# Kernel tuning notes

Hardware: AMD Instinct MI355X
Metric: run time of the kernel (lower is better)

## Reference

```python
import jax, jax.numpy as jnp
import numpy as np

NUM_GRAPHS = 1024

def setup_inputs() -> dict:
    key = jax.random.key(0)
    ks = jax.random.split(key, 6)
    N, E = 500000, 16000000
    x = jax.random.normal(ks[0], (N, 4), dtype=jnp.float32)
    edge_index = jax.random.randint(ks[1], (2, E), 0, N, dtype=jnp.int32)
    batch = jnp.sort(jax.random.randint(ks[2], (N,), 0, NUM_GRAPHS, dtype=jnp.int32))
    eps = jnp.zeros((), dtype=jnp.float32)
    W1 = jax.random.normal(ks[3], (4, 16), dtype=jnp.float32) * 0.5
    b1 = jnp.zeros((16,), dtype=jnp.float32)
    W2 = jax.random.normal(ks[4], (16, 4), dtype=jnp.float32) * 0.25
    b2 = jnp.zeros((4,), dtype=jnp.float32)
    return {"x": x, "edge_index": edge_index, "batch": batch,
            "eps": eps, "W1": W1, "b1": b1, "W2": W2, "b2": b2}

def reference(x, edge_index, batch, eps, W1, b1, W2, b2):
    N = x.shape[0]
    src, dst = edge_index[0], edge_index[1]
    # GINConv aggregation: sum of neighbor (source) features at each target node
    agg = jax.ops.segment_sum(x[src], dst, num_segments=N)  # [N, 4]
    h = (1.0 + eps) * x + agg
    # 2-layer MLP: Lin(4,16) -> ReLU -> Lin(16,4)
    h = jax.nn.relu(h @ W1 + b1) @ W2 + b2
    h = jax.nn.relu(h)
    # global_mean_pool over batch segment ids
    sums = jax.ops.segment_sum(h, batch, num_segments=NUM_GRAPHS)      # [G, 4]
    cnts = jax.ops.segment_sum(jnp.ones((N,), h.dtype), batch, num_segments=NUM_GRAPHS)
    pooled = sums / jnp.maximum(cnts, 1.0)[:, None]
    return jax.nn.log_softmax(pooled, axis=1)
```

## Files before the change

kernel.cpp:

```cpp
#include <hip/hip_runtime.h>

#define NUM_GRAPHS 1024
#define BIN_BITS 10
#define BIN_SIZE (1 << BIN_BITS)
#define EB 8192
#define STH 512
#define EPT 16
#define ATH 1024
#define ACH 8192
#define AEPT (ACH / ATH)

typedef int v4i __attribute__((ext_vector_type(4)));

__device__ inline unsigned bf16_rn(float f) {
    unsigned u = __float_as_uint(f);
    return (u + 0x7FFFu + ((u >> 16) & 1u)) >> 16;
}
__global__ void prep_kernel(const float4* __restrict__ x, uint2* __restrict__ x16,
                            int N, int* __restrict__ cursor,
                            float* __restrict__ gsum, float* __restrict__ gcnt,
                            int cap) {
    int i = blockIdx.x * blockDim.x + threadIdx.x;
    if (i < 512) cursor[i] = i * cap;
    if (i < NUM_GRAPHS * 4) gsum[i] = 0.0f;
    if (i < NUM_GRAPHS) gcnt[i] = 0.0f;
    if (i < N) {
        float4 v = x[i];
        uint2 r;
        r.x = bf16_rn(v.x) | (bf16_rn(v.y) << 16);
        r.y = bf16_rn(v.z) | (bf16_rn(v.w) << 16);
        x16[i] = r;
    }
}

__global__ void __launch_bounds__(STH) bin_scatter(const int* __restrict__ src,
                                                   const int* __restrict__ dst,
                                                   int* __restrict__ packed,
                                                   int* __restrict__ cursor,
                                                   int E, int cap, int nb) {
    __shared__ int shist[512];
    __shared__ int sprefix[513];
    __shared__ int sgbase[512];
    __shared__ int spacked[EB];
    __shared__ unsigned short sbin[EB];
    __shared__ int wsum[8];

    const int t = threadIdx.x;
    const int lane = t & 63;
    const int wave = t >> 6;
    const int b0 = blockIdx.x * EB;
    const int myBase = b0 + t * EPT;

    for (int j = t; j < 512; j += STH) shist[j] = 0;
    __syncthreads();

    int pv[EPT];
    int bl[EPT];
    const bool full = (myBase + EPT <= E);
    if (full) {
#pragma unroll
        for (int v = 0; v < EPT / 4; ++v) {
            int4 d = *(const int4*)(dst + myBase + v * 4);
            int4 s = *(const int4*)(src + myBase + v * 4);
            int bn, lp;
            bn = ((unsigned)d.x) >> BIN_BITS; lp = atomicAdd(&shist[bn], 1);
            pv[v * 4 + 0] = ((d.x & (BIN_SIZE - 1)) << 19) | s.x;
            bl[v * 4 + 0] = (bn << 13) | lp;
            bn = ((unsigned)d.y) >> BIN_BITS; lp = atomicAdd(&shist[bn], 1);
            pv[v * 4 + 1] = ((d.y & (BIN_SIZE - 1)) << 19) | s.y;
            bl[v * 4 + 1] = (bn << 13) | lp;
            bn = ((unsigned)d.z) >> BIN_BITS; lp = atomicAdd(&shist[bn], 1);
            pv[v * 4 + 2] = ((d.z & (BIN_SIZE - 1)) << 19) | s.z;
            bl[v * 4 + 2] = (bn << 13) | lp;
            bn = ((unsigned)d.w) >> BIN_BITS; lp = atomicAdd(&shist[bn], 1);
            pv[v * 4 + 3] = ((d.w & (BIN_SIZE - 1)) << 19) | s.w;
            bl[v * 4 + 3] = (bn << 13) | lp;
        }
    } else {
#pragma unroll
        for (int i = 0; i < EPT; ++i) {
            int e = myBase + i;
            bool ok = e < E;
            int d = ok ? dst[e] : 0;
            int s = ok ? src[e] : 0;
            int bn = ((unsigned)d) >> BIN_BITS;
            int lp = 0;
            if (ok) lp = atomicAdd(&shist[bn], 1);
            pv[i] = ((d & (BIN_SIZE - 1)) << 19) | s;
            bl[i] = ok ? ((bn << 13) | lp) : -1;
        }
    }
    __syncthreads();

    {
        int v = shist[t];
        int inc = v;
#pragma unroll
        for (int off = 1; off < 64; off <<= 1) {
            int u = __shfl_up(inc, off);
            if (lane >= off) inc += u;
        }
        if (lane == 63) wsum[wave] = inc;
        __syncthreads();
        if (t == 0) {
            int acc = 0;
#pragma unroll
            for (int w = 0; w < 8; ++w) { int c = wsum[w]; wsum[w] = acc; acc += c; }
        }
        __syncthreads();
        sprefix[t + 1] = inc + wsum[wave];
        if (t == 0) sprefix[0] = 0;
        if (t < nb && v > 0) sgbase[t] = atomicAdd(&cursor[t], v);
    }
    __syncthreads();

    if (full) {
#pragma unroll
        for (int i = 0; i < EPT; ++i) {
            int bn = ((unsigned)bl[i]) >> 13;
            int lp = bl[i] & 0x1FFF;
            int idx = sprefix[bn] + lp;
            spacked[idx] = pv[i];
            sbin[idx] = (unsigned short)bn;
        }
    } else {
#pragma unroll
        for (int i = 0; i < EPT; ++i) {
            if (bl[i] >= 0) {
                int bn = ((unsigned)bl[i]) >> 13;
                int lp = bl[i] & 0x1FFF;
                int idx = sprefix[bn] + lp;
                spacked[idx] = pv[i];
                sbin[idx] = (unsigned short)bn;
            }
        }
    }
    __syncthreads();

    int cnt = sprefix[nb < 512 ? nb : 512];
    int totE = E - b0; if (totE < 0) totE = 0;
    if (cnt > totE) cnt = totE;
    for (int j = t; j < cnt; j += STH) {
        int bn = sbin[j];
        int pos = sgbase[bn] + (j - sprefix[bn]);
        if (pos < (bn + 1) * cap)
            __builtin_nontemporal_store(spacked[j], &packed[pos]);
    }
}

__global__ void __launch_bounds__(ATH) bin_accum_mlp_pool(
        const float4* __restrict__ x,
        const uint2* __restrict__ x16,
        const int* __restrict__ packed,
        const int* __restrict__ cursor,
        const int* __restrict__ batch,
        const float* __restrict__ eps_p,
        const float* __restrict__ W1, const float* __restrict__ b1,
        const float* __restrict__ W2, const float* __restrict__ b2,
        float* __restrict__ gsum, float* __restrict__ gcnt,
        int N, int cap) {
    __shared__ int srt[ACH];
    __shared__ int hist[BIN_SIZE];
    __shared__ int pfx[BIN_SIZE + 1];
    __shared__ int wsum[16];

    const int bin = blockIdx.x;
    const int t = threadIdx.x;
    const int lane = t & 63;
    const int wave = t >> 6;

    const int start = bin * cap;
    int end = cursor[bin];
    if (end > start + cap) end = start + cap;

    float a0 = 0.f, a1 = 0.f, a2 = 0.f, a3 = 0.f;

#pragma unroll 1
    for (int cs = start; cs < end; cs += ACH) {
        int ce = cs + ACH; if (ce > end) ce = end;

        hist[t] = 0;
        __syncthreads();

        int dlp[AEPT];
        int sv[AEPT];
#pragma unroll
        for (int i = 0; i < AEPT / 4; ++i) {
            int ebase = cs + (i * ATH + t) * 4;
            v4i p4;
            if (ebase + 3 < ce) {
                p4 = __builtin_nontemporal_load((const v4i*)(packed + ebase));
            } else {
                p4.x = (ebase + 0 < ce) ? packed[ebase + 0] : 0;
                p4.y = (ebase + 1 < ce) ? packed[ebase + 1] : 0;
                p4.z = (ebase + 2 < ce) ? packed[ebase + 2] : 0;
                p4.w = (ebase + 3 < ce) ? packed[ebase + 3] : 0;
            }
#pragma unroll
            for (int k = 0; k < 4; ++k) {
                int p = (k == 0) ? p4.x : (k == 1) ? p4.y : (k == 2) ? p4.z : p4.w;
                bool ok = (ebase + k) < ce;
                int dl = ((unsigned)p) >> 19;
                int lp = 0;
                if (ok) lp = atomicAdd(&hist[dl], 1);
                dlp[i * 4 + k] = ok ? ((dl << 13) | lp) : -1;
                sv[i * 4 + k] = p & 0x7FFFF;
            }
        }
        __syncthreads();

        {
            int v = hist[t];
            int inc = v;
#pragma unroll
            for (int off = 1; off < 64; off <<= 1) {
                int u = __shfl_up(inc, off);
                if (lane >= off) inc += u;
            }
            if (lane == 63) wsum[wave] = inc;
            __syncthreads();
            if (t == 0) {
                int acc = 0;
#pragma unroll
                for (int w = 0; w < 16; ++w) { int c = wsum[w]; wsum[w] = acc; acc += c; }
            }
            __syncthreads();
            pfx[t + 1] = inc + wsum[wave];
            if (t == 0) pfx[0] = 0;
        }
        __syncthreads();

#pragma unroll
        for (int i = 0; i < AEPT; ++i) {
            if (dlp[i] >= 0) {
                int dl = ((unsigned)dlp[i]) >> 13;
                int lp = dlp[i] & 0x1FFF;
                srt[pfx[dl] + lp] = sv[i];
            }
        }
        __syncthreads();

        int jb = pfx[t], je = pfx[t + 1];
        for (int j = jb; j < je; ++j) {
            uint2 v = x16[srt[j]];
            a0 += __uint_as_float(v.x << 16);
            a1 += __uint_as_float(v.x & 0xFFFF0000u);
            a2 += __uint_as_float(v.y << 16);
            a3 += __uint_as_float(v.y & 0xFFFF0000u);
        }
        __syncthreads();
    }

    int n = bin * BIN_SIZE + t;
    bool valid = n < N;
    float o0 = 0.f, o1 = 0.f, o2 = 0.f, o3 = 0.f;
    int g = -1;
    if (valid) {
        float eps = eps_p[0];
        float4 xv = x[n];
        float h0 = (1.0f + eps) * xv.x + a0;
        float h1 = (1.0f + eps) * xv.y + a1;
        float h2 = (1.0f + eps) * xv.z + a2;
        float h3 = (1.0f + eps) * xv.w + a3;

        float tmp[16];
#pragma unroll
        for (int j = 0; j < 16; ++j) {
            float v = b1[j] + h0 * W1[j] + h1 * W1[16 + j] + h2 * W1[32 + j] + h3 * W1[48 + j];
            tmp[j] = v > 0.0f ? v : 0.0f;
        }
        float o[4];
#pragma unroll
        for (int j = 0; j < 4; ++j) {
            float v = b2[j];
#pragma unroll
            for (int k = 0; k < 16; ++k) v += tmp[k] * W2[k * 4 + j];
            o[j] = v > 0.0f ? v : 0.0f;
        }
        o0 = o[0]; o1 = o[1]; o2 = o[2]; o3 = o[3];
        g = batch[n];
    }

    int g0 = __shfl(g, 0);
    bool uni = __all(g == g0);
    if (uni && g0 >= 0) {
#pragma unroll
        for (int off = 32; off > 0; off >>= 1) {
            o0 += __shfl_down(o0, off);
            o1 += __shfl_down(o1, off);
            o2 += __shfl_down(o2, off);
            o3 += __shfl_down(o3, off);
        }
        if ((t & 63) == 0) {
            unsafeAtomicAdd(&gsum[(size_t)g0 * 4 + 0], o0);
            unsafeAtomicAdd(&gsum[(size_t)g0 * 4 + 1], o1);
            unsafeAtomicAdd(&gsum[(size_t)g0 * 4 + 2], o2);
            unsafeAtomicAdd(&gsum[(size_t)g0 * 4 + 3], o3);
            unsafeAtomicAdd(&gcnt[g0], 64.0f);
        }
    } else if (valid) {
        unsafeAtomicAdd(&gsum[(size_t)g * 4 + 0], o0);
        unsafeAtomicAdd(&gsum[(size_t)g * 4 + 1], o1);
        unsafeAtomicAdd(&gsum[(size_t)g * 4 + 2], o2);
        unsafeAtomicAdd(&gsum[(size_t)g * 4 + 3], o3);
        unsafeAtomicAdd(&gcnt[g], 1.0f);
    }
}

__global__ void pool_softmax_kernel(const float* __restrict__ gsum,
                                    const float* __restrict__ gcnt,
                                    float* __restrict__ out) {
    int g = blockIdx.x * blockDim.x + threadIdx.x;
    if (g >= NUM_GRAPHS) return;
    float c = fmaxf(gcnt[g], 1.0f);
    float p0 = gsum[g * 4 + 0] / c;
    float p1 = gsum[g * 4 + 1] / c;
    float p2 = gsum[g * 4 + 2] / c;
    float p3 = gsum[g * 4 + 3] / c;
    float m = fmaxf(fmaxf(p0, p1), fmaxf(p2, p3));
    float s = expf(p0 - m) + expf(p1 - m) + expf(p2 - m) + expf(p3 - m);
    float lse = m + logf(s);
    out[g * 4 + 0] = p0 - lse;
    out[g * 4 + 1] = p1 - lse;
    out[g * 4 + 2] = p2 - lse;
    out[g * 4 + 3] = p3 - lse;
}

__global__ void edge_scatter_kernel(const float4* __restrict__ x,
                                    const int* __restrict__ src,
                                    const int* __restrict__ dst,
                                    float* __restrict__ agg,
                                    int E) {
    int t = blockIdx.x * blockDim.x + threadIdx.x;
    int e = t * 4;
    if (e + 3 < E) {
        int4 s = *(const int4*)(src + e);
        int4 d = *(const int4*)(dst + e);
        float4 xv;
        xv = x[s.x];
        unsafeAtomicAdd(&agg[(size_t)d.x * 4 + 0], xv.x);
        unsafeAtomicAdd(&agg[(size_t)d.x * 4 + 1], xv.y);
        unsafeAtomicAdd(&agg[(size_t)d.x * 4 + 2], xv.z);
        unsafeAtomicAdd(&agg[(size_t)d.x * 4 + 3], xv.w);
        xv = x[s.y];
        unsafeAtomicAdd(&agg[(size_t)d.y * 4 + 0], xv.x);
        unsafeAtomicAdd(&agg[(size_t)d.y * 4 + 1], xv.y);
        unsafeAtomicAdd(&agg[(size_t)d.y * 4 + 2], xv.z);
        unsafeAtomicAdd(&agg[(size_t)d.y * 4 + 3], xv.w);
        xv = x[s.z];
        unsafeAtomicAdd(&agg[(size_t)d.z * 4 + 0], xv.x);
        unsafeAtomicAdd(&agg[(size_t)d.z * 4 + 1], xv.y);
        unsafeAtomicAdd(&agg[(size_t)d.z * 4 + 2], xv.z);
        unsafeAtomicAdd(&agg[(size_t)d.z * 4 + 3], xv.w);
        xv = x[s.w];
        unsafeAtomicAdd(&agg[(size_t)d.w * 4 + 0], xv.x);
        unsafeAtomicAdd(&agg[(size_t)d.w * 4 + 1], xv.y);
        unsafeAtomicAdd(&agg[(size_t)d.w * 4 + 2], xv.z);
        unsafeAtomicAdd(&agg[(size_t)d.w * 4 + 3], xv.w);
    } else {
        for (int i = e; i < E; ++i) {
            int sv = src[i], dv = dst[i];
            float4 xv = x[sv];
            unsafeAtomicAdd(&agg[(size_t)dv * 4 + 0], xv.x);
            unsafeAtomicAdd(&agg[(size_t)dv * 4 + 1], xv.y);
            unsafeAtomicAdd(&agg[(size_t)dv * 4 + 2], xv.z);
            unsafeAtomicAdd(&agg[(size_t)dv * 4 + 3], xv.w);
        }
    }
}

__global__ void node_mlp_pool_kernel(const float4* __restrict__ x,
                                     const float4* __restrict__ agg,
                                     const int* __restrict__ batch,
                                     const float* __restrict__ eps_p,
                                     const float* __restrict__ W1,
                                     const float* __restrict__ b1,
                                     const float* __restrict__ W2,
                                     const float* __restrict__ b2,
                                     float* __restrict__ gsum,
                                     float* __restrict__ gcnt,
                                     int N) {
    int i = blockIdx.x * blockDim.x + threadIdx.x;
    bool valid = i < N;
    float o0 = 0.f, o1 = 0.f, o2 = 0.f, o3 = 0.f;
    int g = -1;
    if (valid) {
        float eps = eps_p[0];
        float4 xv = x[i];
        float4 av = agg[i];
        float h0 = (1.0f + eps) * xv.x + av.x;
        float h1 = (1.0f + eps) * xv.y + av.y;
        float h2 = (1.0f + eps) * xv.z + av.z;
        float h3 = (1.0f + eps) * xv.w + av.w;
        float tmp[16];
#pragma unroll
        for (int j = 0; j < 16; ++j) {
            float v = b1[j] + h0 * W1[j] + h1 * W1[16 + j] + h2 * W1[32 + j] + h3 * W1[48 + j];
            tmp[j] = v > 0.0f ? v : 0.0f;
        }
        float o[4];
#pragma unroll
        for (int j = 0; j < 4; ++j) {
            float v = b2[j];
#pragma unroll
            for (int k = 0; k < 16; ++k) v += tmp[k] * W2[k * 4 + j];
            o[j] = v > 0.0f ? v : 0.0f;
        }
        o0 = o[0]; o1 = o[1]; o2 = o[2]; o3 = o[3];
        g = batch[i];
    }
    int g0 = __shfl(g, 0);
    bool uni = __all(g == g0);
    if (uni && g0 >= 0) {
#pragma unroll
        for (int off = 32; off > 0; off >>= 1) {
            o0 += __shfl_down(o0, off);
            o1 += __shfl_down(o1, off);
            o2 += __shfl_down(o2, off);
            o3 += __shfl_down(o3, off);
        }
        if ((threadIdx.x & 63) == 0) {
            unsafeAtomicAdd(&gsum[(size_t)g0 * 4 + 0], o0);
            unsafeAtomicAdd(&gsum[(size_t)g0 * 4 + 1], o1);
            unsafeAtomicAdd(&gsum[(size_t)g0 * 4 + 2], o2);
            unsafeAtomicAdd(&gsum[(size_t)g0 * 4 + 3], o3);
            unsafeAtomicAdd(&gcnt[g0], 64.0f);
        }
    } else if (valid) {
        unsafeAtomicAdd(&gsum[(size_t)g * 4 + 0], o0);
        unsafeAtomicAdd(&gsum[(size_t)g * 4 + 1], o1);
        unsafeAtomicAdd(&gsum[(size_t)g * 4 + 2], o2);
        unsafeAtomicAdd(&gsum[(size_t)g * 4 + 3], o3);
        unsafeAtomicAdd(&gcnt[g], 1.0f);
    }
}

extern "C" void kernel_launch(void* const* d_in, const int* in_sizes, int n_in,
                              void* d_out, int out_size, void* d_ws, size_t ws_size,
                              hipStream_t stream) {
    const float* x     = (const float*)d_in[0];
    const int*   ei    = (const int*)d_in[1];
    const int*   batch = (const int*)d_in[2];
    const float* eps   = (const float*)d_in[3];
    const float* W1    = (const float*)d_in[4];
    const float* b1    = (const float*)d_in[5];
    const float* W2    = (const float*)d_in[6];
    const float* b2    = (const float*)d_in[7];

    const int N = in_sizes[0] / 4;
    const int E = in_sizes[1] / 2;
    const int* src = ei;
    const int* dst = ei + (size_t)E;

    const int nb = (N + BIN_SIZE - 1) >> BIN_BITS;
    const int epb = (E + nb - 1) / nb;
    int cap = epb + epb / 8 + 1024;
    cap = (cap + 3) & ~3;

    size_t x16_elems = ((size_t)2 * N + 3) & ~(size_t)3;
    size_t packed_elems = ((size_t)nb * cap + 3) & ~(size_t)3;
    size_t need = (x16_elems + packed_elems + 512 + NUM_GRAPHS * 5) * sizeof(float);

    if (nb <= 512 && N < (1 << 19) && need <= ws_size) {
        uint2* x16    = (uint2*)d_ws;
        int*   packed = (int*)d_ws + x16_elems;
        int*   cursor = packed + packed_elems;
        float* gsum   = (float*)(cursor + 512);
        float* gcnt   = gsum + (size_t)NUM_GRAPHS * 4;

        prep_kernel<<<(N + 511) / 512, 512, 0, stream>>>(
            (const float4*)x, x16, N, cursor, gsum, gcnt, cap);

        int nblocks_e = (E + EB - 1) / EB;
        bin_scatter<<<nblocks_e, STH, 0, stream>>>(src, dst, packed, cursor, E, cap, nb);

        bin_accum_mlp_pool<<<nb, ATH, 0, stream>>>(
            (const float4*)x, (const uint2*)x16, packed, cursor, batch, eps,
            W1, b1, W2, b2, gsum, gcnt, N, cap);

        pool_softmax_kernel<<<(NUM_GRAPHS + 255) / 256, 256, 0, stream>>>(
            gsum, gcnt, (float*)d_out);
    } else {
        float* agg  = (float*)d_ws;
        float* gsum = agg + (size_t)N * 4;
        float* gcnt = gsum + (size_t)NUM_GRAPHS * 4;
        size_t zero_bytes = ((size_t)N * 4 + NUM_GRAPHS * 5) * sizeof(float);
        (void)hipMemsetAsync(d_ws, 0, zero_bytes, stream);

        int e4 = (E + 3) / 4;
        edge_scatter_kernel<<<(e4 + 255) / 256, 256, 0, stream>>>(
            (const float4*)x, src, dst, agg, E);

        node_mlp_pool_kernel<<<(N + 255) / 256, 256, 0, stream>>>(
            (const float4*)x, (const float4*)agg, batch, eps, W1, b1, W2, b2,
            gsum, gcnt, N);

        pool_softmax_kernel<<<(NUM_GRAPHS + 255) / 256, 256, 0, stream>>>(
            gsum, gcnt, (float*)d_out);
    }
}
```

Baseline: 450.1 us.

## Replace LDS atomic counting sort with 2-bit radix sort per chunk

Each chunk of packed edges is now ordered by local destination with a five-pass, 2-bit LSD radix sort in shared memory, using wave shuffles for the prefix scans, instead of building a histogram with LDS atomics and scattering. Per-destination segment starts are then found by a binary search over the sorted keys rather than by a prefix sum of the histogram. The goal is to remove contended shared-memory atomics and the per-thread register arrays. The cost is five scan-and-scatter passes with several barriers each, plus the binary search. Padding keys are set to -1 so they sort to the end and are then clamped off.

Result: slower. 548.4 us (+21.8%).

```diff
diff --git a/kernel.cpp b/kernel.cpp
--- a/kernel.cpp
+++ b/kernel.cpp
@@ -8,7 +8,7 @@
 #define EPT 16
 #define ATH 1024
 #define ACH 8192
-#define AEPT (ACH / ATH)
+#define IPT 8
 
 typedef int v4i __attribute__((ext_vector_type(4)));
 
@@ -159,10 +159,12 @@
         const float* __restrict__ W2, const float* __restrict__ b2,
         float* __restrict__ gsum, float* __restrict__ gcnt,
         int N, int cap) {
-    __shared__ int srt[ACH];
-    __shared__ int hist[BIN_SIZE];
+    __shared__ int bufA[ACH];
+    __shared__ int bufB[ACH];
     __shared__ int pfx[BIN_SIZE + 1];
-    __shared__ int wsum[16];
+    __shared__ int warr[32];
+    __shared__ int wpre[32];
+    __shared__ int gtot[2];
 
     const int bin = blockIdx.x;
     const int t = threadIdx.x;
@@ -178,71 +180,107 @@
 #pragma unroll 1
     for (int cs = start; cs < end; cs += ACH) {
         int ce = cs + ACH; if (ce > end) ce = end;
-
-        hist[t] = 0;
-        __syncthreads();
-
-        int dlp[AEPT];
-        int sv[AEPT];
-#pragma unroll
-        for (int i = 0; i < AEPT / 4; ++i) {
+        const int cnt = ce - cs;
+
+#pragma unroll
+        for (int i = 0; i < IPT / 4; ++i) {
             int ebase = cs + (i * ATH + t) * 4;
             v4i p4;
             if (ebase + 3 < ce) {
                 p4 = __builtin_nontemporal_load((const v4i*)(packed + ebase));
             } else {
-                p4.x = (ebase + 0 < ce) ? packed[ebase + 0] : 0;
-                p4.y = (ebase + 1 < ce) ? packed[ebase + 1] : 0;
-                p4.z = (ebase + 2 < ce) ? packed[ebase + 2] : 0;
-                p4.w = (ebase + 3 < ce) ? packed[ebase + 3] : 0;
-            }
-#pragma unroll
-            for (int k = 0; k < 4; ++k) {
-                int p = (k == 0) ? p4.x : (k == 1) ? p4.y : (k == 2) ? p4.z : p4.w;
-                bool ok = (ebase + k) < ce;
-                int dl = ((unsigned)p) >> 19;
-                int lp = 0;
-                if (ok) lp = atomicAdd(&hist[dl], 1);
-                dlp[i * 4 + k] = ok ? ((dl << 13) | lp) : -1;
-                sv[i * 4 + k] = p & 0x7FFFF;
-            }
+                p4.x = (ebase + 0 < ce) ? packed[ebase + 0] : -1;
+                p4.y = (ebase + 1 < ce) ? packed[ebase + 1] : -1;
+                p4.z = (ebase + 2 < ce) ? packed[ebase + 2] : -1;
+                p4.w = (ebase + 3 < ce) ? packed[ebase + 3] : -1;
+            }
+            *(v4i*)&bufA[ebase - cs] = p4;
         }
         __syncthreads();
 
+#pragma unroll
+        for (int pass = 0; pass < 5; ++pass) {
+            const int shift = 19 + 2 * pass;
+            int* rb = (pass & 1) ? bufB : bufA;
+            int* wb = (pass & 1) ? bufA : bufB;
+
+            v4i k0 = *(const v4i*)&rb[t * IPT];
+            v4i k1 = *(const v4i*)&rb[t * IPT + 4];
+            int k[IPT] = {k0.x, k0.y, k0.z, k0.w, k1.x, k1.y, k1.z, k1.w};
+
+            int c0 = 0, c1 = 0, c2 = 0, c3 = 0;
+            int r[IPT];
+#pragma unroll
+            for (int i = 0; i < IPT; ++i) {
+                int d = (((unsigned)k[i]) >> shift) & 3;
+                int rr;
+                if (d == 0)      { rr = c0; c0++; }
+                else if (d == 1) { rr = c1; c1++; }
+                else if (d == 2) { rr = c2; c2++; }
+                else             { rr = c3; c3++; }
+                r[i] = rr;
+            }
+            int P0 = c0 | (c1 << 16), P1 = c2 | (c3 << 16);
+            int s0 = P0, s1 = P1;
+#pragma unroll
+            for (int off = 1; off < 64; off <<= 1) {
+                int u0 = __shfl_up(s0, off);
+                int u1 = __shfl_up(s1, off);
+                if (lane >= off) { s0 += u0; s1 += u1; }
+            }
+            if (lane == 63) { warr[wave * 2] = s0; warr[wave * 2 + 1] = s1; }
+            int e0 = s0 - P0, e1 = s1 - P1;
+            __syncthreads();
+
+            if (wave == 0 && lane < 16) {
+                int v0 = warr[lane * 2], v1 = warr[lane * 2 + 1];
+                int t0 = v0, t1 = v1;
+#pragma unroll
+                for (int off = 1; off < 16; off <<= 1) {
+                    int u0 = __shfl_up(t0, off);
+                    int u1 = __shfl_up(t1, off);
+                    if (lane >= off) { t0 += u0; t1 += u1; }
+                }
+                wpre[lane * 2] = t0 - v0;
+                wpre[lane * 2 + 1] = t1 - v1;
+                if (lane == 15) { gtot[0] = t0; gtot[1] = t1; }
+            }
+            __syncthreads();
+
+            int w0 = wpre[wave * 2], w1 = wpre[wave * 2 + 1];
+            int T0 = gtot[0], T1 = gtot[1];
+            int tot0 = T0 & 0xFFFF, tot1 = (T0 >> 16) & 0xFFFF, tot2 = T1 & 0xFFFF;
+            int g0 = 0                   + (w0 & 0xFFFF)         + (e0 & 0xFFFF);
+            int g1 = tot0                + ((w0 >> 16) & 0xFFFF) + ((e0 >> 16) & 0xFFFF);
+            int g2 = tot0 + tot1         + (w1 & 0xFFFF)         + (e1 & 0xFFFF);
+            int g3 = tot0 + tot1 + tot2  + ((w1 >> 16) & 0xFFFF) + ((e1 >> 16) & 0xFFFF);
+#pragma unroll
+            for (int i = 0; i < IPT; ++i) {
+                int d = (((unsigned)k[i]) >> shift) & 3;
+                int base = (d == 0) ? g0 : (d == 1) ? g1 : (d == 2) ? g2 : g3;
+                wb[base + r[i]] = k[i];
+            }
+            __syncthreads();
+        }
+
         {
-            int v = hist[t];
-            int inc = v;
-#pragma unroll
-            for (int off = 1; off < 64; off <<= 1) {
-                int u = __shfl_up(inc, off);
-                if (lane >= off) inc += u;
-            }
-            if (lane == 63) wsum[wave] = inc;
-            __syncthreads();
-            if (t == 0) {
-                int acc = 0;
-#pragma unroll
-                for (int w = 0; w < 16; ++w) { int c = wsum[w]; wsum[w] = acc; acc += c; }
-            }
-            __syncthreads();
-            pfx[t + 1] = inc + wsum[wave];
-            if (t == 0) pfx[0] = 0;
+            int lo = 0, hi = ACH;
+            while (lo < hi) {
+                int mid = (lo + hi) >> 1;
+                int dl = (((unsigned)bufB[mid]) >> 19) & 0x3FF;
+                if (dl < t) lo = mid + 1; else hi = mid;
+            }
+            pfx[t] = lo;
+            if (t == 0) pfx[BIN_SIZE] = ACH;
         }
         __syncthreads();
 
-#pragma unroll
-        for (int i = 0; i < AEPT; ++i) {
-            if (dlp[i] >= 0) {
-                int dl = ((unsigned)dlp[i]) >> 13;
-                int lp = dlp[i] & 0x1FFF;
-                srt[pfx[dl] + lp] = sv[i];
-            }
-        }
-        __syncthreads();
-
-        int jb = pfx[t], je = pfx[t + 1];
+        int jb = pfx[t];
+        int je = pfx[t + 1];
+        if (je > cnt) je = cnt;
         for (int j = jb; j < je; ++j) {
-            uint2 v = x16[srt[j]];
+            int s = bufB[j] & 0x7FFFF;
+            uint2 v = x16[s];
             a0 += __uint_as_float(v.x << 16);
             a1 += __uint_as_float(v.x & 0xFFFF0000u);
             a2 += __uint_as_float(v.y << 16);
```
